# Performance work log

Hardware: AMD Instinct MI355X
Metric: run time of the kernel (lower is better)

## Reference

```python
import jax, jax.numpy as jnp
import numpy as np

B, C, N, L = 32, 256, 1024, 12
H = 8
DK = C // H  # 32


def setup_inputs() -> dict:
    key = jax.random.key(0)
    ks = jax.random.split(key, 8)
    inp = {
        "input": jax.random.normal(ks[0], (B, C, N, L), dtype=jnp.float32),
        # 1x1 conv weights stored as [out_ch, in_ch] (kernel is 1x1)
        "q_w": jax.random.normal(ks[1], (C, C), dtype=jnp.float32) * 0.02,
        "q_b": jnp.zeros((C,), dtype=jnp.float32),
        "v_w": jax.random.normal(ks[2], (C, C), dtype=jnp.float32) * 0.02,
        "v_b": jnp.zeros((C,), dtype=jnp.float32),
        "c_w": jax.random.normal(ks[3], (C, C), dtype=jnp.float32) * 0.02,
        "c_b": jnp.zeros((C,), dtype=jnp.float32),
        # xavier_uniform_: bound = sqrt(6/(fan_in+fan_out)) over last two dims
        "s_bank": jax.random.uniform(ks[4], (H, L, N, DK), dtype=jnp.float32,
                                      minval=-1.0, maxval=1.0) * np.float32(np.sqrt(6.0 / (N + DK))),
    }
    return inp


def _conv1x1_relu(x, w, b):
    # x: [B, Cin, N, L], w: [Cout, Cin] -> [B, Cout, N, L]; dropout is eval-mode identity
    return jax.nn.relu(jnp.einsum('oi,binl->bonl', w, x) + b[None, :, None, None])


def reference(input, q_w, q_b, v_w, v_b, c_w, c_b, s_bank):
    b, c, n, l = input.shape
    inv_sqrt_dk = np.float32(1.0 / np.sqrt(DK))

    q = _conv1x1_relu(input, q_w, q_b)   # [B, C, N, L]
    v = _conv1x1_relu(input, v_w, v_b)   # [B, C, N, L]

    def split_heads(t):
        # [B, C, N, L] -> [B, H, DK, N, L] -> [B, H, L, N, DK]
        return t.reshape(b, H, DK, n, l).transpose(0, 1, 4, 3, 2)

    query = jax.nn.softmax(split_heads(q) * inv_sqrt_dk, axis=-1)        # [B,H,L,N,DK]
    value = split_heads(v)                                               # [B,H,L,N,DK]
    key_ = jax.nn.softmax(s_bank[:, :, :n, :] * inv_sqrt_dk, axis=-1)    # [H,L,N,DK]

    kv = jnp.einsum('hlnx,bhlny->bhlxy', key_, value)      # [B,H,L,DK,DK]
    qkv = jnp.einsum('bhlnx,bhlxy->bhlny', query, kv)      # [B,H,L,N,DK]

    # [B,H,L,N,DK] -> [B,H,DK,N,L] -> [B,C,N,L]
    out = qkv.transpose(0, 1, 4, 3, 2).reshape(b, c, n, l)
    return _conv1x1_relu(out, c_w, c_b)
```

## Files before the change

### kernel.cpp

```cpp
#include <hip/hip_runtime.h>

#define B_   32
#define C_   256
#define N_   1024
#define L_   12
#define H_   8
#define DK_  32
#define NL_  12288
#define CNL_ 3145728
#define ND_  32768
#define HLN_ 98304
#define SCALE_ 0.17677669529663687f

typedef _Float16 half8 __attribute__((ext_vector_type(8)));
typedef _Float16 half4 __attribute__((ext_vector_type(4)));
typedef float f32x4 __attribute__((ext_vector_type(4)));

__device__ __forceinline__ int div12(int s) { return (int)(((unsigned)s * 43691u) >> 19); }

__global__ __launch_bounds__(256) void k_prep(const float* __restrict__ wq,
    const float* __restrict__ wv, const float* __restrict__ cw,
    _Float16* __restrict__ Wfrag, _Float16* __restrict__ Cfrag) {
    const int gid = blockIdx.x * 256 + threadIdx.x;
    if (gid < 16384) {
        const int kb = gid >> 11, r = gid & 2047;
        const int mt = r >> 6, o = (r >> 4) & 3, lo = r & 15;
        const int m = mt * 16 + lo;
        const float* src = (m < 256 ? wq + (size_t)m * 256 : wv + (size_t)(m - 256) * 256)
                           + kb * 32 + o * 8;
        f32x4 a0 = *(const f32x4*)src, a1 = *(const f32x4*)(src + 4);
        half8 h;
#pragma unroll
        for (int i = 0; i < 4; ++i) { h[i] = (_Float16)a0[i]; h[4 + i] = (_Float16)a1[i]; }
        *(half8*)(Wfrag + (size_t)gid * 8) = h;
    } else {
        const int c = gid - 16384;
        const int kb = c >> 10, r = c & 1023;
        const int mt = r >> 6, o = (r >> 4) & 3, lo = r & 15;
        const int m = mt * 16 + lo;
        const float* src = cw + (size_t)m * 256 + kb * 32 + o * 8;
        f32x4 a0 = *(const f32x4*)src, a1 = *(const f32x4*)(src + 4);
        half8 h;
#pragma unroll
        for (int i = 0; i < 4; ++i) { h[i] = (_Float16)a0[i]; h[4 + i] = (_Float16)a1[i]; }
        *(half8*)(Cfrag + (size_t)c * 8) = h;
    }
}

__global__ __launch_bounds__(256) void k_key_softmax(const float* __restrict__ sb,
                                                     _Float16* __restrict__ ksT) {
    __shared__ _Float16 smT[32 * 260];
    const int t = threadIdx.x;
    const int row = blockIdx.x * 256 + t;
    const f32x4* src = (const f32x4*)(sb + (size_t)row * DK_);
    float v[DK_];
#pragma unroll
    for (int i = 0; i < 8; i++) {
        f32x4 t4 = src[i];
        v[4*i+0] = t4[0]; v[4*i+1] = t4[1]; v[4*i+2] = t4[2]; v[4*i+3] = t4[3];
    }
    float m = v[0];
#pragma unroll
    for (int i = 1; i < DK_; i++) m = fmaxf(m, v[i]);
    float s = 0.f;
#pragma unroll
    for (int i = 0; i < DK_; i++) { v[i] = __expf((v[i] - m) * SCALE_); s += v[i]; }
    const float inv = 1.f / s;
#pragma unroll
    for (int i = 0; i < DK_; i++) smT[i * 260 + t] = (_Float16)(v[i] * inv);
    __syncthreads();
    const int x = t >> 3, off = (t & 7) * 32;
    const int base = blockIdx.x * 256;
    const int hl = base >> 10, nb = base & 1023;
    _Float16* dst = ksT + (size_t)hl * ND_ + (size_t)x * 1024 + nb + off;
    const _Float16* srcT = &smT[x * 260 + off];
#pragma unroll
    for (int k = 0; k < 4; ++k)
        *(half8*)(dst + k * 8) = *(const half8*)(srcT + k * 8);
}

__global__ __launch_bounds__(512, 2) void k_conv_qv(
    const float* __restrict__ x, const _Float16* __restrict__ Wfrag,
    const float* __restrict__ bqp, const float* __restrict__ bvp,
    _Float16* __restrict__ qh, _Float16* __restrict__ vh)
{
    __shared__ __align__(16) _Float16 Xl[2][8192];

    const int t = threadIdx.x;
    const int sgrp = blockIdx.x;
    const int b = blockIdx.y;
    const int sbase = sgrp * 768;
    const int w = t >> 6, lane = t & 63;
    const int lo = lane & 15, hi = lane >> 4;

    half8 af[8][4];
#pragma unroll
    for (int kb = 0; kb < 8; ++kb)
#pragma unroll
        for (int m = 0; m < 4; ++m)
            af[kb][m] = *(const half8*)(Wfrag +
                ((size_t)kb*2048 + (size_t)(w*4 + m)*64 + lane) * 8);

    const float* bsel = (w >= 4) ? bvp : bqp;
    f32x4 bb[4];
#pragma unroll
    for (int m = 0; m < 4; ++m)
        bb[m] = *(const f32x4*)(bsel + ((w & 3)*4 + m)*16 + hi*4);

    const int xch = t >> 1, xsh = (t & 1) * 8;
    const int g = xch >> 3, elem = xch & 7;
    const int wb = g*128 + elem;
    const int sx = xsh ^ ((g & 7) << 1) ^ (xsh >> 3);
    const float* px = x + (size_t)b * CNL_ + (size_t)xch * NL_ + sbase + xsh;

    const int base_r = hi*128 + ((lo ^ (hi*2) ^ ((lo & 8) >> 3)) << 3);

    f32x4 c0 = *(const f32x4*)px,        c1 = *(const f32x4*)(px + 4);
    f32x4 c2 = *(const f32x4*)(px + 16), c3 = *(const f32x4*)(px + 20);
#pragma unroll
    for (int k = 0; k < 4; ++k) {
        Xl[0][wb + (((k  ) ^ sx) << 3)]        = (_Float16)c0[k];
        Xl[0][wb + (((k+4) ^ sx) << 3)]        = (_Float16)c1[k];
        Xl[0][4096 + wb + (((k  ) ^ sx) << 3)] = (_Float16)c2[k];
        Xl[0][4096 + wb + (((k+4) ^ sx) << 3)] = (_Float16)c3[k];
    }
    c0 = *(const f32x4*)(px + 32); c1 = *(const f32x4*)(px + 36);
    c2 = *(const f32x4*)(px + 48); c3 = *(const f32x4*)(px + 52);

    for (int i = 0; i < 24; ++i) {
        asm volatile("s_waitcnt lgkmcnt(0)" ::: "memory");
        __builtin_amdgcn_s_barrier();
        __builtin_amdgcn_sched_barrier(0);
        const _Float16* Xc = Xl[i & 1];
        f32x4 acc[4][2] = {};
#pragma unroll
        for (int kb = 0; kb < 8; ++kb) {
            const int ro = kb*512 + (base_r ^ ((kb & 1) << 6));
            half8 bf0 = *(const half8*)&Xc[ro];
            half8 bf1 = *(const half8*)&Xc[4096 + ro];
#pragma unroll
            for (int m = 0; m < 4; ++m) {
                acc[m][0] = __builtin_amdgcn_mfma_f32_16x16x32_f16(af[kb][m], bf0, acc[m][0], 0, 0, 0);
                acc[m][1] = __builtin_amdgcn_mfma_f32_16x16x32_f16(af[kb][m], bf1, acc[m][1], 0, 0, 0);
            }
        }
        if (i < 23) {
            _Float16* Xn = Xl[(i + 1) & 1];
#pragma unroll
            for (int k = 0; k < 4; ++k) {
                Xn[wb + (((k  ) ^ sx) << 3)]        = (_Float16)c0[k];
                Xn[wb + (((k+4) ^ sx) << 3)]        = (_Float16)c1[k];
                Xn[4096 + wb + (((k  ) ^ sx) << 3)] = (_Float16)c2[k];
                Xn[4096 + wb + (((k+4) ^ sx) << 3)] = (_Float16)c3[k];
            }
            if (i < 22) {
                const float* p = px + (size_t)(i + 2) * 32;
                c0 = *(const f32x4*)p;        c1 = *(const f32x4*)(p + 4);
                c2 = *(const f32x4*)(p + 16); c3 = *(const f32x4*)(p + 20);
            }
        }
#pragma unroll
        for (int u = 0; u < 2; ++u) {
            const int sg = sbase + i*32 + u*16 + lo;
            const int n = div12(sg), l = sg - n*12;
#pragma unroll
            for (int m = 0; m < 4; ++m) {
                const int o = (w*4 + m)*16 + hi*4;
                const int ol = o & 255;
                _Float16* dst0 = (w >= 4) ? vh : qh;
                half4 hh;
#pragma unroll
                for (int r = 0; r < 4; ++r) hh[r] = (_Float16)fmaxf(acc[m][u][r] + bb[m][r], 0.f);
                *(half4*)(dst0 + ((size_t)(b*8 + (ol >> 5))*12 + l)*ND_ + (size_t)n*32 + (ol & 31)) = hh;
            }
        }
    }
}

__global__ __launch_bounds__(256) void k_kv(const _Float16* __restrict__ ksT,
    const _Float16* __restrict__ v, _Float16* __restrict__ kvT) {
    __shared__ float red[4096];
    const int bid = blockIdx.x;
    const int bh = bid / 12;
    const int l  = bid - bh * 12;
    const int h  = bh & 7;
    const int t = threadIdx.x, w = t >> 6, lane = t & 63;
    const int lo = lane & 15, hi = lane >> 4;
    const _Float16* vb  = v   + (size_t)bid * ND_;
    const _Float16* ksb = ksT + (size_t)(h*12 + l) * ND_;

    f32x4 acc[2][2] = {};
#pragma unroll 2
    for (int c = 0; c < 8; ++c) {
        const int n0 = w*256 + c*32 + hi*8;
        half8 a0, a1;
#pragma unroll
        for (int j = 0; j < 8; ++j) {
            a0[j] = vb[(size_t)(n0 + j)*32 + lo];
            a1[j] = vb[(size_t)(n0 + j)*32 + 16 + lo];
        }
        half8 b0 = *(const half8*)(ksb + (size_t)lo*1024 + n0);
        half8 b1 = *(const half8*)(ksb + (size_t)(16 + lo)*1024 + n0);
        acc[0][0] = __builtin_amdgcn_mfma_f32_16x16x32_f16(a0, b0, acc[0][0], 0, 0, 0);
        acc[0][1] = __builtin_amdgcn_mfma_f32_16x16x32_f16(a0, b1, acc[0][1], 0, 0, 0);
        acc[1][0] = __builtin_amdgcn_mfma_f32_16x16x32_f16(a1, b0, acc[1][0], 0, 0, 0);
        acc[1][1] = __builtin_amdgcn_mfma_f32_16x16x32_f16(a1, b1, acc[1][1], 0, 0, 0);
    }
#pragma unroll
    for (int m = 0; m < 2; ++m)
#pragma unroll
        for (int xm = 0; xm < 2; ++xm)
#pragma unroll
            for (int reg = 0; reg < 4; ++reg)
                red[w*1024 + (m*16 + hi*4 + reg)*32 + xm*16 + lo] = acc[m][xm][reg];
    __syncthreads();
    const int e = t * 4;
    f32x4 s = *(const f32x4*)&red[e];
    s += *(const f32x4*)&red[1024 + e];
    s += *(const f32x4*)&red[2048 + e];
    s += *(const f32x4*)&red[3072 + e];
    half4 o;
#pragma unroll
    for (int i = 0; i < 4; ++i) o[i] = (_Float16)s[i];
    *(half4*)(kvT + (size_t)bid * 1024 + e) = o;
}

__global__ __launch_bounds__(512, 2) void k_conv_out(
    const _Float16* __restrict__ q, const _Float16* __restrict__ kvw,
    const _Float16* __restrict__ Cfrag, const float* __restrict__ cbp,
    float* __restrict__ out) {
    __shared__ __align__(16) _Float16 Xt[2][3072];
    __shared__ float Cb[256];

    const int t = threadIdx.x;
    const int bx = blockIdx.x, b = blockIdx.y;
    const int s0 = bx * 96;
    const int n0 = bx * 8;
    const int w = t >> 6, lane = t & 63;
    const int lo = lane & 15, hi = lane >> 4;
    if (t < 64) *(f32x4*)&Cb[t*4] = *(const f32x4*)(cbp + t*4);

    f32x4 acc[4][3] = {};

    const bool pvw = (w < 6);
    const int li0 = w * 2;
    const int qrow = n0 + (lo & 7);
    const float rowmask = (lo < 8) ? 1.f : 0.f;
    const size_t hstep = (size_t)12 * ND_;
    const _Float16* qb_b = q + (size_t)b * 8 * hstep;
    const _Float16* kv_b = kvw + (size_t)b * 98304;

    half8 hq0 = {}, hq1 = {};
    if (pvw) {
        hq0 = *(const half8*)(qb_b + (size_t)li0 * ND_ + (size_t)qrow*32 + hi*8);
        hq1 = *(const half8*)(qb_b + (size_t)(li0+1) * ND_ + (size_t)qrow*32 + hi*8);
    }

    for (int ph = 0; ph <= 8; ++ph) {
        if (ph < 8 && pvw) {
            half8 nq0 = hq0, nq1 = hq1;
            if (ph < 7) {
                nq0 = *(const half8*)(qb_b + (ph+1)*hstep + (size_t)li0 * ND_ + (size_t)qrow*32 + hi*8);
                nq1 = *(const half8*)(qb_b + (ph+1)*hstep + (size_t)(li0+1) * ND_ + (size_t)qrow*32 + hi*8);
            }
            const _Float16* kvh = kv_b + (size_t)ph * 12288;
            _Float16* Xd = Xt[ph & 1];
#pragma unroll
            for (int sub = 0; sub < 2; ++sub) {
                const half8 hq = sub ? hq1 : hq0;
                const int li = li0 + sub;
                float qv[8];
#pragma unroll
                for (int i = 0; i < 8; ++i) qv[i] = (float)hq[i];
                float m8 = fmaxf(fmaxf(fmaxf(qv[0], qv[1]), fmaxf(qv[2], qv[3])),
                                 fmaxf(fmaxf(qv[4], qv[5]), fmaxf(qv[6], qv[7])));
                m8 = fmaxf(m8, __shfl_xor(m8, 16));
                m8 = fmaxf(m8, __shfl_xor(m8, 32));
                const float mS = m8 * SCALE_;
                float ex[8]; float ssum = 0.f;
#pragma unroll
                for (int i = 0; i < 8; ++i) { ex[i] = __expf(qv[i]*SCALE_ - mS); ssum += ex[i]; }
                ssum += __shfl_xor(ssum, 16);
                ssum += __shfl_xor(ssum, 32);
                const float pin = rowmask / ssum;
                half8 af;
#pragma unroll
                for (int i = 0; i < 8; ++i) af[i] = (_Float16)(ex[i] * pin);
                const half8 b0 = *(const half8*)(kvh + li*1024 + lo*32 + hi*8);
                const half8 b1 = *(const half8*)(kvh + li*1024 + (16+lo)*32 + hi*8);
                f32x4 d0 = {}, d1 = {};
                d0 = __builtin_amdgcn_mfma_f32_16x16x32_f16(af, b0, d0, 0, 0, 0);
                d1 = __builtin_amdgcn_mfma_f32_16x16x32_f16(af, b1, d1, 0, 0, 0);
                if (hi < 2) {
#pragma unroll
                    for (int reg = 0; reg < 4; ++reg) {
                        const int s = (hi*4 + reg)*12 + li;
                        const int cb_ = (s >> 4)*64 + (s & 15);
                        Xd[(cb_ + (lo >> 3)*16)*8 + (lo & 7)]       = (_Float16)d0[reg];
                        Xd[(cb_ + (2 + (lo >> 3))*16)*8 + (lo & 7)] = (_Float16)d1[reg];
                    }
                }
            }
            hq0 = nq0; hq1 = nq1;
        }
        if (ph >= 1) {
            const _Float16* Wk = Cfrag + (size_t)(ph - 1) * 8192;
            const _Float16* Xc = Xt[(ph - 1) & 1];
            half8 af2[4], bf[3];
#pragma unroll
            for (int m = 0; m < 4; ++m)
                af2[m] = *(const half8*)(Wk + ((((w>>1)*4 + m)*4 + hi)*16 + lo) * 8);
#pragma unroll
            for (int sf = 0; sf < 3; ++sf)
                bf[sf] = *(const half8*)&Xc[((((w&1)*3 + sf)*4 + hi)*16 + lo) * 8];
#pragma unroll
            for (int m = 0; m < 4; ++m)
#pragma unroll
                for (int sf = 0; sf < 3; ++sf)
                    acc[m][sf] = __builtin_amdgcn_mfma_f32_16x16x32_f16(af2[m], bf[sf], acc[m][sf], 0, 0, 0);
        }
        asm volatile("s_waitcnt lgkmcnt(0)" ::: "memory");
        __builtin_amdgcn_s_barrier();
        __builtin_amdgcn_sched_barrier(0);
    }

#pragma unroll
    for (int m = 0; m < 4; ++m) {
        const int o = (w>>1)*64 + m*16 + hi*4;
        const f32x4 bb = *(const f32x4*)&Cb[o];
#pragma unroll
        for (int sf = 0; sf < 3; ++sf) {
            const int s = s0 + (w&1)*48 + sf*16 + lo;
            float* dst = out + (size_t)(b*256 + o)*12288 + s;
#pragma unroll
            for (int i = 0; i < 4; ++i)
                dst[(size_t)i * 12288] = fmaxf(acc[m][sf][i] + bb[i], 0.f);
        }
    }
}

extern "C" void kernel_launch(void* const* d_in, const int* in_sizes, int n_in,
                              void* d_out, int out_size, void* d_ws, size_t ws_size,
                              hipStream_t stream) {
    const float* input = (const float*)d_in[0];
    const float* q_w   = (const float*)d_in[1];
    const float* q_b   = (const float*)d_in[2];
    const float* v_w   = (const float*)d_in[3];
    const float* v_b   = (const float*)d_in[4];
    const float* c_w   = (const float*)d_in[5];
    const float* c_b   = (const float*)d_in[6];
    const float* s_bank= (const float*)d_in[7];
    float* out = (float*)d_out;

    char* ws = (char*)d_ws;
    _Float16* ks16 = (_Float16*)ws;
    _Float16* qh   = (_Float16*)(ws + 6291456);
    _Float16* vh   = qh + (size_t)100663296;
    _Float16* kvT  = vh + (size_t)100663296;
    _Float16* Wfrag= kvT + (size_t)3145728;
    _Float16* Cfrag= Wfrag + (size_t)131072;

    k_prep<<<dim3(96), dim3(256), 0, stream>>>(q_w, v_w, c_w, Wfrag, Cfrag);
    k_key_softmax<<<dim3(HLN_ / 256), dim3(256), 0, stream>>>(s_bank, ks16);
    k_conv_qv<<<dim3(16, 32), dim3(512), 0, stream>>>(input, Wfrag, q_b, v_b, qh, vh);
    k_kv<<<dim3(B_ * H_ * L_), dim3(256), 0, stream>>>(ks16, vh, kvT);
    k_conv_out<<<dim3(128, 32), dim3(512), 0, stream>>>(qh, kvT, Cfrag, c_b, out);
}
```

Before: 563.2 us.

## Process two heads per phase in conv_out to halve barrier count

The output-conv kernel now handles two heads per pipeline phase instead of one. All 8 waves share the 24 (head, l) units, three each, instead of 6 waves doing two. The LDS staging buffer doubles so both heads' kv products can be double-buffered, and each phase runs two rounds of conv MFMAs. This cuts the loop from 9 to 5 barrier phases and removes the two idle waves in the attention stage. The cost is more LDS per block and more registers per wave, which may reduce occupancy.

```diff
diff --git a/kernel.cpp b/kernel.cpp
--- a/kernel.cpp
+++ b/kernel.cpp
@@ -229,7 +229,7 @@
     const _Float16* __restrict__ q, const _Float16* __restrict__ kvw,
     const _Float16* __restrict__ Cfrag, const float* __restrict__ cbp,
     float* __restrict__ out) {
-    __shared__ __align__(16) _Float16 Xt[2][3072];
+    __shared__ __align__(16) _Float16 Xt[2][2][3072];
     __shared__ float Cb[256];
 
     const int t = threadIdx.x;
@@ -242,36 +242,46 @@
 
     f32x4 acc[4][3] = {};
 
-    const bool pvw = (w < 6);
-    const int li0 = w * 2;
     const int qrow = n0 + (lo & 7);
     const float rowmask = (lo < 8) ? 1.f : 0.f;
     const size_t hstep = (size_t)12 * ND_;
     const _Float16* qb_b = q + (size_t)b * 8 * hstep;
     const _Float16* kv_b = kvw + (size_t)b * 98304;
 
-    half8 hq0 = {}, hq1 = {};
-    if (pvw) {
-        hq0 = *(const half8*)(qb_b + (size_t)li0 * ND_ + (size_t)qrow*32 + hi*8);
-        hq1 = *(const half8*)(qb_b + (size_t)(li0+1) * ND_ + (size_t)qrow*32 + hi*8);
-    }
-
-    for (int ph = 0; ph <= 8; ++ph) {
-        if (ph < 8 && pvw) {
-            half8 nq0 = hq0, nq1 = hq1;
-            if (ph < 7) {
-                nq0 = *(const half8*)(qb_b + (ph+1)*hstep + (size_t)li0 * ND_ + (size_t)qrow*32 + hi*8);
-                nq1 = *(const half8*)(qb_b + (ph+1)*hstep + (size_t)(li0+1) * ND_ + (size_t)qrow*32 + hi*8);
-            }
-            const _Float16* kvh = kv_b + (size_t)ph * 12288;
-            _Float16* Xd = Xt[ph & 1];
-#pragma unroll
-            for (int sub = 0; sub < 2; ++sub) {
-                const half8 hq = sub ? hq1 : hq0;
-                const int li = li0 + sub;
+    int uhp[3], uli[3];
+#pragma unroll
+    for (int s = 0; s < 3; ++s) {
+        const int u = w*3 + s;
+        uhp[s] = (u >= 12) ? 1 : 0;
+        uli[s] = u - uhp[s]*12;
+    }
+
+    half8 hq[3];
+#pragma unroll
+    for (int s = 0; s < 3; ++s)
+        hq[s] = *(const half8*)(qb_b + (size_t)(0*2 + uhp[s])*hstep
+                                + (size_t)uli[s]*ND_ + (size_t)qrow*32 + hi*8);
+
+    for (int p = 0; p <= 4; ++p) {
+        if (p < 4) {
+            half8 nq[3];
+#pragma unroll
+            for (int s = 0; s < 3; ++s) nq[s] = hq[s];
+            if (p < 3) {
+#pragma unroll
+                for (int s = 0; s < 3; ++s)
+                    nq[s] = *(const half8*)(qb_b + (size_t)((p+1)*2 + uhp[s])*hstep
+                                            + (size_t)uli[s]*ND_ + (size_t)qrow*32 + hi*8);
+            }
+#pragma unroll
+            for (int s = 0; s < 3; ++s) {
+                const half8 hqv = hq[s];
+                const int li = uli[s];
+                const _Float16* kvh = kv_b + (size_t)(p*2 + uhp[s]) * 12288;
+                _Float16* Xd = Xt[p & 1][uhp[s]];
                 float qv[8];
 #pragma unroll
-                for (int i = 0; i < 8; ++i) qv[i] = (float)hq[i];
+                for (int i = 0; i < 8; ++i) qv[i] = (float)hqv[i];
                 float m8 = fmaxf(fmaxf(fmaxf(qv[0], qv[1]), fmaxf(qv[2], qv[3])),
                                  fmaxf(fmaxf(qv[4], qv[5]), fmaxf(qv[6], qv[7])));
                 m8 = fmaxf(m8, __shfl_xor(m8, 16));
@@ -283,41 +293,45 @@
                 ssum += __shfl_xor(ssum, 16);
                 ssum += __shfl_xor(ssum, 32);
                 const float pin = rowmask / ssum;
-                half8 af;
-#pragma unroll
-                for (int i = 0; i < 8; ++i) af[i] = (_Float16)(ex[i] * pin);
+                half8 afp;
+#pragma unroll
+                for (int i = 0; i < 8; ++i) afp[i] = (_Float16)(ex[i] * pin);
                 const half8 b0 = *(const half8*)(kvh + li*1024 + lo*32 + hi*8);
                 const half8 b1 = *(const half8*)(kvh + li*1024 + (16+lo)*32 + hi*8);
                 f32x4 d0 = {}, d1 = {};
-                d0 = __builtin_amdgcn_mfma_f32_16x16x32_f16(af, b0, d0, 0, 0, 0);
-                d1 = __builtin_amdgcn_mfma_f32_16x16x32_f16(af, b1, d1, 0, 0, 0);
+                d0 = __builtin_amdgcn_mfma_f32_16x16x32_f16(afp, b0, d0, 0, 0, 0);
+                d1 = __builtin_amdgcn_mfma_f32_16x16x32_f16(afp, b1, d1, 0, 0, 0);
                 if (hi < 2) {
 #pragma unroll
                     for (int reg = 0; reg < 4; ++reg) {
-                        const int s = (hi*4 + reg)*12 + li;
-                        const int cb_ = (s >> 4)*64 + (s & 15);
+                        const int sr = (hi*4 + reg)*12 + li;
+                        const int cb_ = (sr >> 4)*64 + (sr & 15);
                         Xd[(cb_ + (lo >> 3)*16)*8 + (lo & 7)]       = (_Float16)d0[reg];
                         Xd[(cb_ + (2 + (lo >> 3))*16)*8 + (lo & 7)] = (_Float16)d1[reg];
                     }
                 }
             }
-            hq0 = nq0; hq1 = nq1;
-        }
-        if (ph >= 1) {
-            const _Float16* Wk = Cfrag + (size_t)(ph - 1) * 8192;
-            const _Float16* Xc = Xt[(ph - 1) & 1];
-            half8 af2[4], bf[3];
-#pragma unroll
-            for (int m = 0; m < 4; ++m)
-                af2[m] = *(const half8*)(Wk + ((((w>>1)*4 + m)*4 + hi)*16 + lo) * 8);
-#pragma unroll
-            for (int sf = 0; sf < 3; ++sf)
-                bf[sf] = *(const half8*)&Xc[((((w&1)*3 + sf)*4 + hi)*16 + lo) * 8];
-#pragma unroll
-            for (int m = 0; m < 4; ++m)
+#pragma unroll
+            for (int s = 0; s < 3; ++s) hq[s] = nq[s];
+        }
+        if (p >= 1) {
+#pragma unroll
+            for (int h01 = 0; h01 < 2; ++h01) {
+                const _Float16* Wk = Cfrag + (size_t)((p-1)*2 + h01) * 8192;
+                const _Float16* Xc = Xt[(p - 1) & 1][h01];
+                half8 af2[4], bf[3];
+#pragma unroll
+                for (int m = 0; m < 4; ++m)
+                    af2[m] = *(const half8*)(Wk + ((((w>>1)*4 + m)*4 + hi)*16 + lo) * 8);
 #pragma unroll
                 for (int sf = 0; sf < 3; ++sf)
-                    acc[m][sf] = __builtin_amdgcn_mfma_f32_16x16x32_f16(af2[m], bf[sf], acc[m][sf], 0, 0, 0);
+                    bf[sf] = *(const half8*)&Xc[((((w&1)*3 + sf)*4 + hi)*16 + lo) * 8];
+#pragma unroll
+                for (int m = 0; m < 4; ++m)
+#pragma unroll
+                    for (int sf = 0; sf < 3; ++sf)
+                        acc[m][sf] = __builtin_amdgcn_mfma_f32_16x16x32_f16(af2[m], bf[sf], acc[m][sf], 0, 0, 0);
+            }
         }
         asm volatile("s_waitcnt lgkmcnt(0)" ::: "memory");
         __builtin_amdgcn_s_barrier();
```

Result: slower. 636.1 us (+12.9%).
